# Performance work log

Hardware: AMD Instinct MI355X
Metric: run time of the kernel (lower is better)

## Reference

```python
import jax, jax.numpy as jnp
import numpy as np

F_DIM, H, B, MAX = 128, 256, 256, 128
N = B * MAX            # 32768 nodes, 256 graphs of 128 nodes each
E = 524288             # avg degree 16
EPS = 1e-5


def _bn(x, g, b):
    # BatchNorm1d in training mode: biased batch stats over the node axis
    m = x.mean(0)
    v = x.var(0)
    return (x - m) * jax.lax.rsqrt(v + EPS) * g + b


def _gcn(x, W, b, src, dst, n):
    # PyG GCNConv: add self-loops, symmetric deg^-1/2 normalization
    h = x @ W
    loops = jnp.arange(n, dtype=src.dtype)
    s = jnp.concatenate([src, loops])
    d = jnp.concatenate([dst, loops])
    deg = jax.ops.segment_sum(jnp.ones_like(s, dtype=x.dtype), d, num_segments=n)
    dinv = jax.lax.rsqrt(jnp.maximum(deg, 1.0))
    norm = dinv[s] * dinv[d]
    out = jax.ops.segment_sum(h[s] * norm[:, None], d, num_segments=n)
    return out + b


def setup_inputs() -> dict:
    key = jax.random.key(0)
    ks = jax.random.split(key, 20)

    def xavier(k, shape, gain=1.414):
        lim = gain * np.sqrt(6.0 / (shape[0] + shape[1]))
        return jax.random.uniform(k, shape, jnp.float32, -lim, lim)

    inp = {}
    inp['x'] = jax.random.normal(ks[0], (N, F_DIM), jnp.float32)
    inp['src_local'] = jax.random.randint(ks[1], (E,), 0, MAX, jnp.int32)
    inp['dst_local'] = jax.random.randint(ks[2], (E,), 0, MAX, jnp.int32)
    dims = [(F_DIM, H), (H, H), (H, H)]
    for i, (di, do) in enumerate(dims):
        inp[f'gcn_w{i}'] = xavier(ks[3 + i], (di, do))
        inp[f'gcn_b{i}'] = jnp.zeros((do,), jnp.float32)
        inp[f'bn_g{i}'] = jnp.ones((do,), jnp.float32)
        inp[f'bn_b{i}'] = jnp.zeros((do,), jnp.float32)
    inp['sc_w0'] = xavier(ks[6], (F_DIM, H), 1.0)
    inp['sc_b0'] = jnp.zeros((H,), jnp.float32)
    inp['edge_w'] = xavier(ks[7], (H, H), 0.01)
    inp['fd_w0'] = xavier(ks[8], (H, H)); inp['fd_b0'] = jnp.zeros((H,), jnp.float32)
    inp['fd_g0'] = jnp.ones((H,), jnp.float32); inp['fd_be0'] = jnp.zeros((H,), jnp.float32)
    inp['fd_w1'] = xavier(ks[9], (H, H)); inp['fd_b1'] = jnp.zeros((H,), jnp.float32)
    inp['fd_g1'] = jnp.ones((H,), jnp.float32); inp['fd_be1'] = jnp.zeros((H,), jnp.float32)
    inp['fd_w2'] = xavier(ks[10], (H, F_DIM)); inp['fd_b2'] = jnp.zeros((F_DIM,), jnp.float32)
    inp['ph_w0'] = xavier(ks[11], (H, H)); inp['ph_b0'] = jnp.zeros((H,), jnp.float32)
    inp['ph_w1'] = xavier(ks[12], (H, H)); inp['ph_b1'] = jnp.zeros((H,), jnp.float32)
    return inp


def reference(x, src_local, dst_local,
              gcn_w0, gcn_b0, bn_g0, bn_b0, sc_w0, sc_b0,
              gcn_w1, gcn_b1, bn_g1, bn_b1,
              gcn_w2, gcn_b2, bn_g2, bn_b2,
              edge_w,
              fd_w0, fd_b0, fd_g0, fd_be0,
              fd_w1, fd_b1, fd_g1, fd_be1,
              fd_w2, fd_b2,
              ph_w0, ph_b0, ph_w1, ph_b1):
    n = x.shape[0]
    # global edge index: edge e belongs to graph e // (E//B); offset by g*MAX
    off = (jnp.arange(E, dtype=jnp.int32) // (E // B)) * MAX
    src = src_local + off
    dst = dst_local + off

    def block(h, W, b, g, bb, shortcut):
        res = shortcut(h)
        out = jax.nn.relu(_bn(_gcn(h, W, b, src, dst, n), g, bb))
        return jax.nn.relu(out + res)  # dropout is identity at inference

    z = block(x, gcn_w0, gcn_b0, bn_g0, bn_b0, lambda h: h @ sc_w0 + sc_b0)
    z = block(z, gcn_w1, gcn_b1, bn_g1, bn_b1, lambda h: h)
    z = block(z, gcn_w2, gcn_b2, bn_g2, bn_b2, lambda h: h)
    # F.normalize(p=2, dim=1)
    z = z / jnp.maximum(jnp.linalg.norm(z, axis=1, keepdims=True), 1e-12)

    # BilinearEdgeDecoder per graph, vectorized: sigmoid(Z W Z^T) with zero diag
    zb = z.reshape(B, MAX, H)
    adj = jax.nn.sigmoid(jnp.einsum('bnd,de,bme->bnm', zb, edge_w, zb))
    adj = adj * (1.0 - jnp.eye(MAX, dtype=adj.dtype))

    # Feature_Decoder: [Linear,ReLU,BN] x2 then Linear
    h = _bn(jax.nn.relu(z @ fd_w0 + fd_b0), fd_g0, fd_be0)
    h = _bn(jax.nn.relu(h @ fd_w1 + fd_b1), fd_g1, fd_be1)
    x_recon = h @ fd_w2 + fd_b2

    z_g = zb.max(axis=1)  # global_max_pool per graph
    z_g_mlp = jax.nn.relu(z_g @ ph_w0 + ph_b0) @ ph_w1 + ph_b1
    return (z, adj, x_recon, z_g, z_g_mlp)
```

## Files before the change

### kernel.cpp

```cpp
#include <hip/hip_runtime.h>
#include <hip/hip_bf16.h>

using bf = __hip_bfloat16;
typedef __attribute__((ext_vector_type(8))) short s8;
typedef __attribute__((ext_vector_type(4))) float f4;

constexpr int NN  = 32768;
constexpr int HD  = 256;

__device__ __forceinline__ float u2f(unsigned short h) {
    union { unsigned u; float f; } x; x.u = ((unsigned)h) << 16;
    return x.f;
}
__device__ __forceinline__ unsigned short f2u(float f) {
    union { float f; unsigned u; } x; x.f = f;
    unsigned r = x.u + 0x7FFF + ((x.u >> 16) & 1);
    return (unsigned short)(r >> 16);
}
__device__ __forceinline__ bf f2bf(float f) {
    unsigned short h = f2u(f);
    return *reinterpret_cast<bf*>(&h);
}
__device__ __forceinline__ float bf2f(bf b) {
    return u2f(*reinterpret_cast<unsigned short*>(&b));
}

__device__ __forceinline__ int swz(int row, int slot) {
    return row * 64 + ((slot ^ (row & 7)) << 3);
}
__device__ __forceinline__ int swz128(int row, int slot) {
    return row * 128 + ((slot ^ (row & 7)) << 3);
}

__global__ __launch_bounds__(256) void k_adj(const int* __restrict__ srcL,
                                             const int* __restrict__ dstL,
                                             bf* __restrict__ A) {
    __shared__ float sT[128 * 64];
    __shared__ float sdin[128];
    int g = blockIdx.x, t = threadIdx.x;
    const int* sg = srcL + (g << 11);
    const int* dg = dstL + (g << 11);
    if (t < 128) sdin[t] = 0.f;
    __syncthreads();
    for (int e = t; e < 2048; e += 256) atomicAdd(&sdin[dg[e]], 1.0f);
    __syncthreads();
    if (t < 128) sdin[t] = rsqrtf(sdin[t] + 1.0f);
    __syncthreads();
    bf* out = A + ((long)g << 14);
    for (int half = 0; half < 2; ++half) {
        for (int i = t; i < 8192; i += 256) sT[i] = 0.f;
        __syncthreads();
        for (int e = t; e < 2048; e += 256) {
            int s = sg[e], d = dg[e];
            if ((s >> 6) == half)
                atomicAdd(&sT[(d << 6) + (s & 63)], sdin[s] * sdin[d]);
        }
        __syncthreads();
        if (t < 128 && (t >> 6) == half)
            sT[(t << 6) + (t & 63)] += sdin[t] * sdin[t];
        __syncthreads();
        for (int i4 = t; i4 < 2048; i4 += 256) {
            int d = i4 >> 4, c4 = (i4 & 15) * 4;
            float4 v = *(float4*)&sT[(d << 6) + c4];
            ushort4 u = make_ushort4(f2u(v.x), f2u(v.y), f2u(v.z), f2u(v.w));
            *(ushort4*)&out[(d << 7) + (half << 6) + c4] = u;
        }
        __syncthreads();
    }
}

struct WTd { const float* src; int K, N, off; };
struct WTpack { WTd w[10]; };
__global__ void k_wt(WTpack p, bf* __restrict__ out) {
    WTd d = p.w[blockIdx.z];
    int n0 = blockIdx.x * 64, k0 = blockIdx.y * 64;
    if (n0 >= d.N || k0 >= d.K) return;
    __shared__ float s[64][65];
    int t = threadIdx.x;
    int cc = t & 63, rq = t >> 6;
#pragma unroll
    for (int i = 0; i < 16; ++i) {
        int r = i * 4 + rq;
        s[r][cc] = d.src[(long)(k0 + r) * d.N + n0 + cc];
    }
    __syncthreads();
#pragma unroll
    for (int i = 0; i < 16; ++i) {
        int r = i * 4 + rq;
        out[d.off + (long)(n0 + r) * d.K + k0 + cc] = f2bf(s[cc][r]);
    }
}

template <int EPI, int OUT, bool PART, bool BNA>
__global__ __launch_bounds__(256) void mg(
    const bf* __restrict__ A, const bf* __restrict__ BT,
    const float* __restrict__ bias, const float* __restrict__ bnstats,
    float* __restrict__ Cf, bf* __restrict__ Cb, float* __restrict__ part,
    int M, int N, int K, int ldc) {
    __shared__ __align__(16) bf sAl[128 * 64];
    __shared__ __align__(16) bf sBl[128 * 64];
    const int m0 = blockIdx.y * 128, n0 = blockIdx.x * 128;
    const bf* Ab = A + (long)m0 * K;
    const bf* Bb = BT + (long)n0 * K;
    const int t = threadIdx.x;
    const int lane = t & 63;
    const int w = t >> 6;
    const int wm = (w >> 1) * 64, wn = (w & 1) * 64;
    const int fr16 = lane & 15, kq = lane >> 4;
    f4 acc[4][4] = {};
    for (int k0 = 0; k0 < K; k0 += 64) {
#pragma unroll
        for (int i = 0; i < 4; ++i) {
            int sdx = i * 256 + t;
            int row = sdx >> 3, sl = sdx & 7;
            s8 av = *(const s8*)&Ab[(long)row * K + k0 + sl * 8];
            if constexpr (BNA) {
                int c = k0 + sl * 8;
                float4 sc0 = *(const float4*)&bnstats[c];
                float4 sc1 = *(const float4*)&bnstats[c + 4];
                float4 sh0 = *(const float4*)&bnstats[256 + c];
                float4 sh1 = *(const float4*)&bnstats[256 + c + 4];
                float scv[8] = {sc0.x, sc0.y, sc0.z, sc0.w, sc1.x, sc1.y, sc1.z, sc1.w};
                float shv[8] = {sh0.x, sh0.y, sh0.z, sh0.w, sh1.x, sh1.y, sh1.z, sh1.w};
                unsigned short* u = (unsigned short*)&av;
#pragma unroll
                for (int j = 0; j < 8; ++j)
                    u[j] = f2u(fmaf(u2f(u[j]), scv[j], shv[j]));
            }
            *(s8*)&sAl[swz(row, sl)] = av;
            *(s8*)&sBl[swz(row, sl)] = *(const s8*)&Bb[(long)row * K + k0 + sl * 8];
        }
        __syncthreads();
#pragma unroll
        for (int ks = 0; ks < 2; ++ks) {
            s8 af[4], bg[4];
#pragma unroll
            for (int f = 0; f < 4; ++f) {
                af[f] = *(const s8*)&sAl[swz(wm + f * 16 + fr16, kq + 4 * ks)];
                bg[f] = *(const s8*)&sBl[swz(wn + f * 16 + fr16, kq + 4 * ks)];
            }
#pragma unroll
            for (int fr = 0; fr < 4; ++fr)
#pragma unroll
                for (int fc = 0; fc < 4; ++fc)
                    acc[fr][fc] = __builtin_amdgcn_mfma_f32_16x16x32_bf16(
                        af[fr], bg[fc], acc[fr][fc], 0, 0, 0);
        }
        __syncthreads();
    }
    float ps[4], ps2[4];
    if (PART) {
#pragma unroll
        for (int fc = 0; fc < 4; ++fc) { ps[fc] = 0.f; ps2[fc] = 0.f; }
    }
#pragma unroll
    for (int fr = 0; fr < 4; ++fr) {
        int rl = wm + fr * 16 + (lane >> 4) * 4;
#pragma unroll
        for (int fc = 0; fc < 4; ++fc) {
            int cl = wn + fc * 16 + (lane & 15);
            int col = n0 + cl;
            float bv = bias[col];
#pragma unroll
            for (int i = 0; i < 4; ++i) {
                float v = acc[fr][fc][i] + bv;
                if (EPI == 2) v = fmaxf(v, 0.f);
                if (PART) { ps[fc] += v; ps2[fc] += v * v; }
                if (OUT == 0) Cf[(long)(m0 + rl + i) * ldc + col] = v;
                if (OUT == 1) Cb[(long)(m0 + rl + i) * ldc + col] = f2bf(v);
            }
        }
    }
    if (PART) {
        __syncthreads();
        float* scr = (float*)sAl;
#pragma unroll
        for (int fc = 0; fc < 4; ++fc) {
            ps[fc] += __shfl_xor(ps[fc], 16);  ps[fc] += __shfl_xor(ps[fc], 32);
            ps2[fc] += __shfl_xor(ps2[fc], 16); ps2[fc] += __shfl_xor(ps2[fc], 32);
        }
        if (lane < 16) {
#pragma unroll
            for (int fc = 0; fc < 4; ++fc) {
                scr[(w * 2 + 0) * 64 + fc * 16 + lane] = ps[fc];
                scr[(w * 2 + 1) * 64 + fc * 16 + lane] = ps2[fc];
            }
        }
        __syncthreads();
        int id = blockIdx.x * gridDim.y + blockIdx.y;
        int stat = t >> 7, c = t & 127;
        int ci = c & 63, half = c >> 6;
        float v = scr[(half * 2 + stat) * 64 + ci] + scr[((half + 2) * 2 + stat) * 64 + ci];
        part[(long)id * 256 + stat * 128 + c] = v;
    }
}

template <int MODE>
__global__ __launch_bounds__(512) void k_fused(
    const bf* __restrict__ Xin, const float* __restrict__ xf,
    const bf* __restrict__ Res, const float* __restrict__ stats,
    const bf* __restrict__ Wt, const bf* __restrict__ Wt2,
    const float* __restrict__ scb, const bf* __restrict__ Adj,
    bf* __restrict__ Zout, bf* __restrict__ AG, bf* __restrict__ ResOut,
    float* __restrict__ part, float* __restrict__ adjout) {
    __shared__ __align__(16) bf sOut[128 * 128];
    __shared__ __align__(16) bf sStg[128 * 128];
    const int g = blockIdx.x;
    const int hb = blockIdx.y;
    const int t = threadIdx.x;
    const int lane = t & 63, w = t >> 6;
    const int wm = w >> 2, wn = w & 3;
    const int l15 = lane & 15, kq = lane >> 4;
    constexpr int KS1 = (MODE == 2) ? 128 : 256;
    const int h0 = (MODE == 1) ? 0 : hb;
    const int h1 = (MODE == 1) ? 2 : hb + 1;
    const bf* Xg = (MODE != 2) ? Xin + (long)g * 32768 : nullptr;
    const bf* Rg = (MODE == 0) ? Res + (long)g * 32768 : nullptr;
    f4 acc2[4][2] = {};
    for (int h = h0; h < h1; ++h) {
        f4 acc1[4][2] = {};
        for (int k0 = 0; k0 < KS1; k0 += 64) {
            __syncthreads();
#pragma unroll
            for (int i = 0; i < 2; ++i) {
                int sdx = i * 512 + t;
                int row = sdx >> 3, sl = sdx & 7;
                int c = k0 + sl * 8;
                s8 av;
                if constexpr (MODE == 0) {
                    av = *(const s8*)&Xg[row * 256 + c];
                    s8 rv = *(const s8*)&Rg[row * 256 + c];
                    float4 sc0 = *(const float4*)&stats[c];
                    float4 sc1 = *(const float4*)&stats[c + 4];
                    float4 sh0 = *(const float4*)&stats[256 + c];
                    float4 sh1 = *(const float4*)&stats[256 + c + 4];
                    float scv[8] = {sc0.x, sc0.y, sc0.z, sc0.w, sc1.x, sc1.y, sc1.z, sc1.w};
                    float shv[8] = {sh0.x, sh0.y, sh0.z, sh0.w, sh1.x, sh1.y, sh1.z, sh1.w};
                    unsigned short* u = (unsigned short*)&av;
                    const unsigned short* ru = (const unsigned short*)&rv;
#pragma unroll
                    for (int j = 0; j < 8; ++j) {
                        float v = fmaf(u2f(u[j]), scv[j], shv[j]);
                        v = fmaxf(v, 0.f) + u2f(ru[j]);
                        u[j] = f2u(fmaxf(v, 0.f));
                    }
                    if (h == 0)
                        *(s8*)&Zout[(long)g * 32768 + row * 256 + c] = av;
                } else if constexpr (MODE == 2) {
                    const float* src = xf + ((long)(g * 128 + row)) * 128 + c;
                    float4 f0 = *(const float4*)src;
                    float4 f1 = *(const float4*)(src + 4);
                    unsigned short u[8] = {f2u(f0.x), f2u(f0.y), f2u(f0.z), f2u(f0.w),
                                           f2u(f1.x), f2u(f1.y), f2u(f1.z), f2u(f1.w)};
                    av = *(s8*)u;
                } else {
                    av = *(const s8*)&Wt[(h * 128 + row) * 256 + c];
                }
                *(s8*)&sStg[swz(row, sl)] = av;
                s8 bv;
                if constexpr (MODE == 0)
                    bv = *(const s8*)&Wt[(h * 128 + row) * 256 + c];
                else if constexpr (MODE == 2) {
                    const bf* Wsrc = (h < 2) ? Wt : Wt2;
                    bv = *(const s8*)&Wsrc[((h & 1) * 128 + row) * 128 + c];
                } else
                    bv = *(const s8*)&Xg[row * 256 + c];
                *(s8*)&sStg[8192 + swz(row, sl)] = bv;
            }
            __syncthreads();
#pragma unroll
            for (int ks = 0; ks < 2; ++ks) {
                s8 af[4], bg[2];
#pragma unroll
                for (int f = 0; f < 4; ++f)
                    af[f] = *(const s8*)&sStg[swz(wm * 64 + f * 16 + l15, kq + 4 * ks)];
#pragma unroll
                for (int f = 0; f < 2; ++f)
                    bg[f] = *(const s8*)&sStg[8192 + swz(wn * 32 + f * 16 + l15, kq + 4 * ks)];
#pragma unroll
                for (int fr = 0; fr < 4; ++fr)
#pragma unroll
                    for (int fc = 0; fc < 2; ++fc)
                        acc1[fr][fc] = __builtin_amdgcn_mfma_f32_16x16x32_bf16(
                            af[fr], bg[fc], acc1[fr][fc], 0, 0, 0);
            }
        }
        if (MODE == 2 && h >= 2) {
#pragma unroll
            for (int fr = 0; fr < 4; ++fr) {
                int rl = wm * 64 + fr * 16 + kq * 4;
#pragma unroll
                for (int fc = 0; fc < 2; ++fc) {
                    int cl = wn * 32 + fc * 16 + l15;
                    float bv = scb[(h - 2) * 128 + cl];
#pragma unroll
                    for (int i = 0; i < 4; ++i)
                        ResOut[(long)(g * 128 + rl + i) * 256 + (h - 2) * 128 + cl] =
                            f2bf(acc1[fr][fc][i] + bv);
                }
            }
            continue;
        }
#pragma unroll
        for (int fr = 0; fr < 4; ++fr) {
            int rl = wm * 64 + fr * 16 + kq * 4;
#pragma unroll
            for (int fc = 0; fc < 2; ++fc) {
                int cl = wn * 32 + fc * 16 + l15;
                ushort4 q = make_ushort4(f2u(acc1[fr][fc][0]), f2u(acc1[fr][fc][1]),
                                         f2u(acc1[fr][fc][2]), f2u(acc1[fr][fc][3]));
                int off = cl * 128 + (((rl >> 3) ^ (cl & 7)) << 3) + (rl & 7);
                *(ushort4*)&sOut[off] = q;
            }
        }
        __syncthreads();
#pragma unroll
        for (int i = 0; i < 4; ++i) {
            int sdx = i * 512 + t;
            int row = sdx >> 4, sl = sdx & 15;
            const bf* src = (MODE == 1)
                ? Xg + row * 256 + h * 128 + sl * 8
                : Adj + ((long)g << 14) + row * 128 + sl * 8;
            *(s8*)&sStg[swz128(row, sl)] = *(const s8*)src;
        }
        __syncthreads();
        if (MODE != 1) {
#pragma unroll
            for (int fr = 0; fr < 4; ++fr)
#pragma unroll
                for (int fc = 0; fc < 2; ++fc) acc2[fr][fc] = f4{0.f, 0.f, 0.f, 0.f};
        }
#pragma unroll
        for (int ks = 0; ks < 4; ++ks) {
            s8 af[4], bg[2];
#pragma unroll
            for (int f = 0; f < 4; ++f)
                af[f] = *(const s8*)&sStg[swz128(wm * 64 + f * 16 + l15, ks * 4 + kq)];
#pragma unroll
            for (int f = 0; f < 2; ++f)
                bg[f] = *(const s8*)&sOut[swz128(wn * 32 + f * 16 + l15, ks * 4 + kq)];
#pragma unroll
            for (int fr = 0; fr < 4; ++fr)
#pragma unroll
                for (int fc = 0; fc < 2; ++fc)
                    acc2[fr][fc] = __builtin_amdgcn_mfma_f32_16x16x32_bf16(
                        af[fr], bg[fc], acc2[fr][fc], 0, 0, 0);
        }
        if (MODE != 1) {
            float ps[2] = {0.f, 0.f}, ps2[2] = {0.f, 0.f};
#pragma unroll
            for (int fr = 0; fr < 4; ++fr) {
                int rl = wm * 64 + fr * 16 + kq * 4;
#pragma unroll
                for (int fc = 0; fc < 2; ++fc) {
                    int cl = wn * 32 + fc * 16 + l15;
#pragma unroll
                    for (int i = 0; i < 4; ++i) {
                        float v = acc2[fr][fc][i];
                        ps[fc] += v; ps2[fc] += v * v;
                        AG[(long)(g * 128 + rl + i) * 256 + h * 128 + cl] = f2bf(v);
                    }
                }
            }
            __syncthreads();
            float* scr = (float*)sStg;
#pragma unroll
            for (int fc = 0; fc < 2; ++fc) {
                ps[fc] += __shfl_xor(ps[fc], 16);  ps[fc] += __shfl_xor(ps[fc], 32);
                ps2[fc] += __shfl_xor(ps2[fc], 16); ps2[fc] += __shfl_xor(ps2[fc], 32);
            }
            if (lane < 16) {
#pragma unroll
                for (int fc = 0; fc < 2; ++fc) {
                    int c = wn * 32 + fc * 16 + lane;
                    scr[(c * 2 + wm) * 2 + 0] = ps[fc];
                    scr[(c * 2 + wm) * 2 + 1] = ps2[fc];
                }
            }
            __syncthreads();
            if (t < 256) {
                int col = t & 127, s = t >> 7;
                part[(long)(h * 256 + g) * 256 + s * 128 + col] =
                    scr[(col * 2 + 0) * 2 + s] + scr[(col * 2 + 1) * 2 + s];
            }
        }
        if (MODE == 1 && h == 1) {
#pragma unroll
            for (int fr = 0; fr < 4; ++fr) {
                int rl = wm * 64 + fr * 16 + kq * 4;
#pragma unroll
                for (int fc = 0; fc < 2; ++fc) {
                    int cl = wn * 32 + fc * 16 + l15;
                    float vv[4];
#pragma unroll
                    for (int i = 0; i < 4; ++i) {
                        float v = 1.f / (1.f + __expf(-acc2[fr][fc][i]));
                        if (cl == rl + i) v = 0.f;
                        vv[i] = v;
                    }
                    float4 o; o.x = vv[0]; o.y = vv[1]; o.z = vv[2]; o.w = vv[3];
                    *(float4*)&adjout[((long)g << 14) + cl * 128 + rl] = o;
                }
            }
        }
    }
}

__global__ void k_bnfin(const float* __restrict__ part, const float* __restrict__ gam,
                        const float* __restrict__ bet, float* __restrict__ stats) {
    int ch = blockIdx.x;
    int half = ch >> 7, cc = ch & 127;
    int t = threadIdx.x;
    __shared__ float2 sm[256];
    const float* p = part + (long)(half * 256 + t) * 256;
    sm[t] = make_float2(p[cc], p[128 + cc]);
    __syncthreads();
    for (int s = 128; s > 0; s >>= 1) {
        if (t < s) { sm[t].x += sm[t + s].x; sm[t].y += sm[t + s].y; }
        __syncthreads();
    }
    if (t == 0) {
        float m = sm[0].x / (float)NN;
        float var = sm[0].y / (float)NN - m * m;
        float sc = rsqrtf(var + 1e-5f) * gam[ch];
        stats[ch]       = sc;
        stats[256 + ch] = bet[ch] - m * sc;
    }
}

__global__ __launch_bounds__(512) void k_finz(
    const bf* __restrict__ X, const float* __restrict__ stats,
    const bf* __restrict__ res, float* __restrict__ outz, bf* __restrict__ Znb,
    float* __restrict__ outzg, bf* __restrict__ ZGb) {
    int g = blockIdx.x, t = threadIdx.x;
    int rr = t >> 8;
    int c = t & 255;
    int lane = t & 63, wid = (t >> 6) & 3;
    float cmax = 0.f;
    __shared__ float red[2][4];
    __shared__ float den[2];
    __shared__ float pm[512];
    for (int it = 0; it < 64; ++it) {
        int r = it * 2 + rr;
        long i = (long)(g * 128 + r) * 256 + c;
        float v = fmaf(bf2f(X[i]), stats[c], stats[256 + c]);
        v = fmaxf(v, 0.f) + bf2f(res[i]);
        v = fmaxf(v, 0.f);
        float s = v * v;
#pragma unroll
        for (int o = 32; o > 0; o >>= 1) s += __shfl_down(s, o);
        if (lane == 0) red[rr][wid] = s;
        __syncthreads();
        if (c == 0) den[rr] = fmaxf(sqrtf(red[rr][0] + red[rr][1] + red[rr][2] + red[rr][3]),
                                    1e-12f);
        __syncthreads();
        float o = v / den[rr];
        outz[i] = o;
        Znb[i] = f2bf(o);
        cmax = fmaxf(cmax, o);
    }
    pm[t] = cmax;
    __syncthreads();
    if (t < 256) {
        float m = fmaxf(pm[t], pm[t + 256]);
        outzg[g * 256 + t] = m;
        ZGb[g * 256 + t] = f2bf(m);
    }
}

template <int EPI, int OUT, bool PART, bool BNA>
static void MG(hipStream_t st, const bf* A, const bf* BT, const float* bias,
               const float* bnstats, float* Cf, bf* Cb, float* part,
               int M, int N, int K, int ldc) {
    dim3 g(N / 128, M / 128, 1);
    mg<EPI, OUT, PART, BNA><<<g, 256, 0, st>>>(A, BT, bias, bnstats, Cf, Cb, part,
                                               M, N, K, ldc);
}

extern "C" void kernel_launch(void* const* d_in, const int* in_sizes, int n_in,
                              void* d_out, int out_size, void* d_ws, size_t ws_size,
                              hipStream_t stream) {
    const float* x      = (const float*)d_in[0];
    const int*   srcL   = (const int*)d_in[1];
    const int*   dstL   = (const int*)d_in[2];
    const float* gcn_w0 = (const float*)d_in[3];
    const float* bn_g0  = (const float*)d_in[5];
    const float* bn_b0  = (const float*)d_in[6];
    const float* gcn_w1 = (const float*)d_in[7];
    const float* bn_g1  = (const float*)d_in[9];
    const float* bn_b1  = (const float*)d_in[10];
    const float* gcn_w2 = (const float*)d_in[11];
    const float* bn_g2  = (const float*)d_in[13];
    const float* bn_b2  = (const float*)d_in[14];
    const float* sc_w0  = (const float*)d_in[15];
    const float* sc_b0  = (const float*)d_in[16];
    const float* edge_w = (const float*)d_in[17];
    const float* fd_w0  = (const float*)d_in[18];
    const float* fd_b0  = (const float*)d_in[19];
    const float* fd_g0  = (const float*)d_in[20];
    const float* fd_be0 = (const float*)d_in[21];
    const float* fd_w1  = (const float*)d_in[22];
    const float* fd_b1  = (const float*)d_in[23];
    const float* fd_g1  = (const float*)d_in[24];
    const float* fd_be1 = (const float*)d_in[25];
    const float* fd_w2  = (const float*)d_in[26];
    const float* fd_b2  = (const float*)d_in[27];
    const float* ph_w0  = (const float*)d_in[28];
    const float* ph_b0  = (const float*)d_in[29];
    const float* ph_w1  = (const float*)d_in[30];
    const float* ph_b1  = (const float*)d_in[31];

    float* out     = (float*)d_out;
    float* out_z   = out;
    float* out_adj = out + 8388608;
    float* out_xr  = out + 12582912;
    float* out_zg  = out + 16777216;
    float* out_zgm = out + 16842752;

    float* w     = (float*)d_ws;
    float* part  = w;
    float* stats = w + 131072;
    bf*    wT    = (bf*)(w + 131584);
    bf*    Aadjb = (bf*)(w + 410112);
    bf*    U4    = (bf*)(w + 2507264);
    bf*    U1    = (bf*)(w + 6701568);
    bf*    U2    = (bf*)(w + 10895872);
    bf*    U3    = (bf*)(w + 15090176);
    bf*    ZGb   = (bf*)(w + 19284480);
    bf*    P1b   = (bf*)(w + 19317248);

    WTpack pk;
    pk.w[0] = {gcn_w0, 128, 256, 0};
    pk.w[1] = {sc_w0,  128, 256, 32768};
    pk.w[2] = {gcn_w1, 256, 256, 65536};
    pk.w[3] = {gcn_w2, 256, 256, 131072};
    pk.w[4] = {edge_w, 256, 256, 196608};
    pk.w[5] = {fd_w0,  256, 256, 262144};
    pk.w[6] = {fd_w1,  256, 256, 327680};
    pk.w[7] = {fd_w2,  256, 128, 393216};
    pk.w[8] = {ph_w0,  256, 256, 425984};
    pk.w[9] = {ph_w1,  256, 256, 491520};

    k_adj<<<256, 256, 0, stream>>>(srcL, dstL, Aadjb);
    k_wt<<<dim3(4, 4, 10), 256, 0, stream>>>(pk, wT);

    k_fused<2><<<dim3(256, 4), 512, 0, stream>>>(nullptr, x, nullptr, nullptr,
                                                 wT + 0, wT + 32768, sc_b0, Aadjb,
                                                 nullptr, U2, U1, part, nullptr);
    k_bnfin<<<256, 256, 0, stream>>>(part, bn_g0, bn_b0, stats);

    k_fused<0><<<dim3(256, 2), 512, 0, stream>>>(U2, nullptr, U1, stats,
                                                 wT + 65536, nullptr, nullptr, Aadjb,
                                                 U3, U4, nullptr, part, nullptr);
    k_bnfin<<<256, 256, 0, stream>>>(part, bn_g1, bn_b1, stats);

    k_fused<0><<<dim3(256, 2), 512, 0, stream>>>(U4, nullptr, U3, stats,
                                                 wT + 131072, nullptr, nullptr, Aadjb,
                                                 U1, U2, nullptr, part, nullptr);
    k_bnfin<<<256, 256, 0, stream>>>(part, bn_g2, bn_b2, stats);

    k_finz<<<256, 512, 0, stream>>>(U2, stats, U1, out_z, U3, out_zg, ZGb);

    k_fused<1><<<dim3(256, 1), 512, 0, stream>>>(U3, nullptr, nullptr, nullptr,
                                                 wT + 196608, nullptr, nullptr, nullptr,
                                                 nullptr, nullptr, nullptr, nullptr,
                                                 out_adj);

    MG<2, 1, true, false>(stream, U3, wT + 262144, fd_b0, nullptr,
                          nullptr, U4, part, NN, HD, HD, 256);
    k_bnfin<<<256, 256, 0, stream>>>(part, fd_g0, fd_be0, stats);
    MG<2, 1, true, true>(stream, U4, wT + 327680, fd_b1, stats,
                         nullptr, U2, part, NN, HD, HD, 256);
    k_bnfin<<<256, 256, 0, stream>>>(part, fd_g1, fd_be1, stats);
    MG<1, 0, false, true>(stream, U2, wT + 393216, fd_b2, stats,
                          out_xr, nullptr, nullptr, NN, 128, HD, 128);

    MG<2, 1, false, false>(stream, ZGb, wT + 425984, ph_b0, nullptr,
                           nullptr, P1b, nullptr, 256, 256, 256, 256);
    MG<1, 0, false, false>(stream, P1b, wT + 491520, ph_b1, nullptr,
                           out_zgm, nullptr, nullptr, 256, 256, 256, 256);
}
```

Measured before the change: 214.3 us.

## Vectorize row-normalize kernel with per-wavefront rows and atomic max pooling

Rewrites the final normalize/max-pool kernel so each 64-lane wavefront owns a whole row with 4 channels per lane. Row norms are reduced with xor shuffles instead of block-wide syncthreads, and loads and stores are vectorized. The grid is split in two halves per graph, which adds a memset, uint atomicMax pooling (valid only because values are non-negative) and a small conversion kernel for the bf16 copy. It targets the barrier-heavy serialized loop in the old kernel, at the cost of two extra launches.

Result: faster. 185.7 us (-13.4%).

```diff
diff --git a/kernel.cpp b/kernel.cpp
--- a/kernel.cpp
+++ b/kernel.cpp
@@ -431,41 +431,65 @@
 __global__ __launch_bounds__(512) void k_finz(
     const bf* __restrict__ X, const float* __restrict__ stats,
     const bf* __restrict__ res, float* __restrict__ outz, bf* __restrict__ Znb,
-    float* __restrict__ outzg, bf* __restrict__ ZGb) {
-    int g = blockIdx.x, t = threadIdx.x;
-    int rr = t >> 8;
-    int c = t & 255;
-    int lane = t & 63, wid = (t >> 6) & 3;
-    float cmax = 0.f;
-    __shared__ float red[2][4];
-    __shared__ float den[2];
-    __shared__ float pm[512];
-    for (int it = 0; it < 64; ++it) {
-        int r = it * 2 + rr;
-        long i = (long)(g * 128 + r) * 256 + c;
-        float v = fmaf(bf2f(X[i]), stats[c], stats[256 + c]);
-        v = fmaxf(v, 0.f) + bf2f(res[i]);
-        v = fmaxf(v, 0.f);
-        float s = v * v;
-#pragma unroll
-        for (int o = 32; o > 0; o >>= 1) s += __shfl_down(s, o);
-        if (lane == 0) red[rr][wid] = s;
-        __syncthreads();
-        if (c == 0) den[rr] = fmaxf(sqrtf(red[rr][0] + red[rr][1] + red[rr][2] + red[rr][3]),
-                                    1e-12f);
-        __syncthreads();
-        float o = v / den[rr];
-        outz[i] = o;
-        Znb[i] = f2bf(o);
-        cmax = fmaxf(cmax, o);
-    }
-    pm[t] = cmax;
+    unsigned* __restrict__ zgu) {
+    int g = blockIdx.x, half = blockIdx.y;
+    int t = threadIdx.x;
+    int lane = t & 63, w = t >> 6;
+    int c4 = lane * 4;
+    float4 sc = *(const float4*)&stats[c4];
+    float4 sh = *(const float4*)&stats[256 + c4];
+    float scv[4] = {sc.x, sc.y, sc.z, sc.w};
+    float shv[4] = {sh.x, sh.y, sh.z, sh.w};
+    float cmax[4] = {0.f, 0.f, 0.f, 0.f};
+#pragma unroll
+    for (int it = 0; it < 8; ++it) {
+        int r = half * 64 + w * 8 + it;
+        long i = (long)(g * 128 + r) * 256 + c4;
+        ushort4 xv = *(const ushort4*)(X + i);
+        ushort4 rv = *(const ushort4*)(res + i);
+        unsigned short xs[4] = {xv.x, xv.y, xv.z, xv.w};
+        unsigned short rs[4] = {rv.x, rv.y, rv.z, rv.w};
+        float v[4];
+        float s = 0.f;
+#pragma unroll
+        for (int j = 0; j < 4; ++j) {
+            float vv = fmaf(u2f(xs[j]), scv[j], shv[j]);
+            vv = fmaxf(vv, 0.f) + u2f(rs[j]);
+            vv = fmaxf(vv, 0.f);
+            v[j] = vv;
+            s += vv * vv;
+        }
+#pragma unroll
+        for (int o = 1; o < 64; o <<= 1) s += __shfl_xor(s, o);
+        float den = fmaxf(sqrtf(s), 1e-12f);
+        float4 fo;
+        unsigned short us[4];
+#pragma unroll
+        for (int j = 0; j < 4; ++j) {
+            float o = v[j] / den;
+            ((float*)&fo)[j] = o;
+            us[j] = f2u(o);
+            cmax[j] = fmaxf(cmax[j], o);
+        }
+        *(float4*)(outz + i) = fo;
+        *(ushort4*)(Znb + i) = make_ushort4(us[0], us[1], us[2], us[3]);
+    }
+    __shared__ float pm[8][256];
+#pragma unroll
+    for (int j = 0; j < 4; ++j) pm[w][c4 + j] = cmax[j];
     __syncthreads();
     if (t < 256) {
-        float m = fmaxf(pm[t], pm[t + 256]);
-        outzg[g * 256 + t] = m;
-        ZGb[g * 256 + t] = f2bf(m);
-    }
+        float m = pm[0][t];
+#pragma unroll
+        for (int ww = 1; ww < 8; ++ww) m = fmaxf(m, pm[ww][t]);
+        atomicMax(&zgu[g * 256 + t], __float_as_uint(m));
+    }
+}
+
+__global__ void k_zgcvt(const float* __restrict__ zg, bf* __restrict__ ZGb) {
+    int i4 = (blockIdx.x * 256 + threadIdx.x) * 4;
+    float4 v = *(const float4*)&zg[i4];
+    *(ushort4*)&ZGb[i4] = make_ushort4(f2u(v.x), f2u(v.y), f2u(v.z), f2u(v.w));
 }
 
 template <int EPI, int OUT, bool PART, bool BNA>
@@ -541,6 +565,8 @@
     pk.w[8] = {ph_w0,  256, 256, 425984};
     pk.w[9] = {ph_w1,  256, 256, 491520};
 
+    hipMemsetAsync(out_zg, 0, 65536 * 4, stream);
+
     k_adj<<<256, 256, 0, stream>>>(srcL, dstL, Aadjb);
     k_wt<<<dim3(4, 4, 10), 256, 0, stream>>>(pk, wT);
 
@@ -559,7 +585,9 @@
                                                  U1, U2, nullptr, part, nullptr);
     k_bnfin<<<256, 256, 0, stream>>>(part, bn_g2, bn_b2, stats);
 
-    k_finz<<<256, 512, 0, stream>>>(U2, stats, U1, out_z, U3, out_zg, ZGb);
+    k_finz<<<dim3(256, 2), 512, 0, stream>>>(U2, stats, U1, out_z, U3,
+                                             (unsigned*)out_zg);
+    k_zgcvt<<<64, 256, 0, stream>>>(out_zg, ZGb);
 
     k_fused<1><<<dim3(256, 1), 512, 0, stream>>>(U3, nullptr, nullptr, nullptr,
                                                  wT + 196608, nullptr, nullptr, nullptr,
```
